# Kernel tuning notes

Hardware: AMD Instinct MI355X
Metric: run time of the kernel (lower is better)

Reference implementation:

```python
import jax, jax.numpy as jnp
import numpy as np

NBIT = 8


def _qmm(x, W, key):
    """Bit-serial quantized matmul with per-bit noisy weights (faithful to torch quantization()).
    x: (..., in), W: (out, in). Returns z (..., out), min, max, last noisy weight."""
    nsplit = 2 ** NBIT - 1
    mn = jnp.min(x)
    mx = jnp.max(x)
    q = ((x - mn) / (mx - mn) * nsplit).astype(jnp.uint8)  # trunc cast like torch .type(uint8)
    z = jnp.zeros(x.shape[:-1] + (W.shape[0],), x.dtype)
    Wn = W
    for i in range(NBIT):  # fixed 8-bit loop
        noise = jax.random.normal(jax.random.fold_in(key, i), W.shape, W.dtype) * jnp.abs(W) * 0.1
        Wn = W + noise
        bit = ((q >> i) & 1).astype(x.dtype) * float(2 ** i)
        z = z + jnp.matmul(bit, Wn.T)
    return z, mn, mx, Wn  # Wn = weight left in fc after loop (last bit's noisy weight)


def _requant(z, mn, mx, W_last):
    nsplit = 2 ** NBIT - 1
    bias = jnp.sum(mn * W_last, axis=1)  # (out,)
    return z / nsplit * (mx - mn) + bias


def _bn(x2d, gamma, beta, eps=1e-5):
    m = x2d.mean(axis=0)
    v = x2d.var(axis=0)  # biased, like torch BN training normalization
    return (x2d - m) / jnp.sqrt(v + eps) * gamma + beta


def _forward(node_embedding, edge_embedding, nbr_mask, c_two, c_two2, c_three, c_three2,
             bn2_g, bn2_b, bn3_g, bn3_b, nbr_idx):
    B, At, Nbr, Fe = edge_embedding.shape
    Fn = node_embedding.shape[-1]
    gather = jax.vmap(lambda x, i: x[i])  # batched fancy gather along atom axis
    key = jax.random.key(42)

    # two-body
    node_i = jnp.broadcast_to(node_embedding[:, :, None, :], (B, At, Nbr, Fn))
    node_j = gather(node_embedding, nbr_idx) * nbr_mask[..., None]  # (B,At,Nbr,Fn)
    c2 = jnp.concatenate([node_i, node_j], axis=3)  # (B,At,Nbr,2Fn)
    z, mn, mx, Wl = _qmm(c2, c_two, jax.random.fold_in(key, 0))
    c2 = jax.nn.relu(_requant(z, mn, mx, Wl))
    z, mn, mx, Wl = _qmm(c2, c_two2, jax.random.fold_in(key, 1))
    c2 = _requant(z, mn, mx, Wl)
    g2, e2 = jnp.split(c2, 2, axis=3)
    two = jax.nn.sigmoid(g2) * jnp.tanh(e2)
    two = _bn(two.reshape(-1, Fe), bn2_g, bn2_b).reshape(B, At, Nbr, Fe)

    # three-body
    nbr_jk = gather(nbr_idx, nbr_idx)                 # (B,At,Nbr,Nbr) neighbors-of-neighbors
    node_k = gather(node_embedding, nbr_jk)           # (B,At,Nbr,Nbr,Fn)
    edge_jk = gather(edge_embedding, nbr_idx)         # (B,At,Nbr,Nbr,Fe)
    edge_ij = jnp.broadcast_to(edge_embedding[:, :, :, None, :], (B, At, Nbr, Nbr, Fe))
    c3 = jnp.concatenate([
        jnp.broadcast_to(node_i[:, :, :, None, :], (B, At, Nbr, Nbr, Fn)),
        jnp.broadcast_to(node_j[:, :, :, None, :], (B, At, Nbr, Nbr, Fn)),
        node_k, edge_ij, edge_jk], axis=4)            # (B,At,Nbr,Nbr,3Fn+2Fe)
    z, mn, mx, Wl = _qmm(c3, c_three, jax.random.fold_in(key, 2))
    c3 = jax.nn.relu(_requant(z, mn, mx, Wl))
    z, mn, mx, Wl = _qmm(c3, c_three2, jax.random.fold_in(key, 3))
    c3 = _requant(z, mn, mx, Wl)
    g3, e3 = jnp.split(c3, 2, axis=4)
    three = jax.nn.sigmoid(g3) * jnp.tanh(e3)
    mask_jk = gather(nbr_mask, nbr_idx)               # (B,At,Nbr,Nbr) = nbr_mask[b, nbr_idx[b,i,j], k]
    three = (three * mask_jk[..., None]).sum(axis=3)  # (B,At,Nbr,Fe)
    three = _bn(three.reshape(-1, Fe), bn3_g, bn3_b).reshape(B, At, Nbr, Fe)

    return jax.nn.relu(edge_embedding + two + three)


def setup_inputs() -> dict:
    key = jax.random.key(0)
    ks = jax.random.split(key, 8)
    B, At, Nbr, Fn, Fe = 4, 48, 20, 64, 64
    return {
        "node_embedding": jax.random.normal(ks[0], (B, At, Fn), jnp.float32),
        "edge_embedding": jax.random.normal(ks[1], (B, At, Nbr, Fe), jnp.float32),
        "nbr_mask": jnp.ones((B, At, Nbr), jnp.float32),
        "c_two": jax.random.normal(ks[2], (8 * Fn, 2 * Fn), jnp.float32) * 0.05,
        "c_two2": jax.random.normal(ks[3], (2 * Fe, 8 * Fn), jnp.float32) * 0.05,
        "c_three": jax.random.normal(ks[4], (6 * Fn + 4 * Fe, 3 * Fn + 2 * Fe), jnp.float32) * 0.05,
        "c_three2": jax.random.normal(ks[5], (2 * Fe, 6 * Fn + 4 * Fe), jnp.float32) * 0.05,
        "bn2_g": jnp.ones((Fe,), jnp.float32),
        "bn2_b": jnp.zeros((Fe,), jnp.float32),
        "bn3_g": jnp.ones((Fe,), jnp.float32),
        "bn3_b": jnp.zeros((Fe,), jnp.float32),
        "nbr_idx": jax.random.randint(ks[6], (B, At, Nbr), 0, At, jnp.int32),
    }


def reference(node_embedding, edge_embedding, nbr_mask, c_two, c_two2, c_three, c_three2,
              bn2_g, bn2_b, bn3_g, bn3_b, nbr_idx):
    return _forward(node_embedding, edge_embedding, nbr_mask, c_two, c_two2, c_three, c_three2,
                    bn2_g, bn2_b, bn3_g, bn3_b, nbr_idx)
```

## Files before the change

### kernel.cpp

```cpp
#include <hip/hip_runtime.h>
#include <cstdint>
#include <cstddef>

#define DEVI __device__ __forceinline__

typedef __attribute__((ext_vector_type(8))) short s8v;
typedef __attribute__((ext_vector_type(4))) float f4v;

static constexpr int B_ = 4, AT = 48, NBRS = 20;
static constexpr int R2 = B_ * AT * NBRS;
static constexpr int M4 = R2 * NBRS;

static constexpr size_t OFF_B2A  = 0;
static constexpr size_t OFF_B2B  = OFF_B2A + 524288;
static constexpr size_t OFF_B3A  = OFF_B2B + 524288;
static constexpr size_t OFF_BW3B = OFF_B3A + 1638400;
static constexpr size_t OFF_BN3B = OFF_BW3B + 81920;
static constexpr size_t OFF_W72A = OFF_BN3B + 327680;
static constexpr size_t OFF_W72B = OFF_W72A + 65536;
static constexpr size_t OFF_W73A = OFF_W72B + 65536;
static constexpr size_t OFF_W73B = OFF_W73A + 204800;
static constexpr size_t OFF_RS   = OFF_W73B + 81920;
static constexpr size_t OFF_SLOT = OFF_RS + 1408;
static constexpr size_t OFF_BN   = OFF_SLOT + 16;
// ... 222 lines not shown
    unsigned char* __restrict__ Q2A, unsigned* __restrict__ slot4) {
  __shared__ float sred[512];
  int idx0 = blockIdx.x * 256 + threadIdx.x;
  if (idx0 < R2 * 128) {
    const float mn = o2f(slot0[0]), mx = o2f(slot0[1]);
    float invd = 255.f / (mx - mn);
    Q2A[idx0] = (unsigned char)((c2in[idx0] - mn) * invd);
  }
  const int n0 = 12288, n1 = n0 + 245760, n2 = n1 + 245760, total = n2 + 4915200;
  float lmn = 3.4e38f, lmx = -3.4e38f;
  for (int idx = idx0; idx < total; idx += gridDim.x * 256) {
    float v, v2;
    if (idx < n0) { v = node[idx]; v2 = v; }
    else if (idx < n1) { v = edge[idx - n0]; v2 = v; }
    else if (idx < n2) {
      int j = idx - n1; int r = j >> 6, c = j & 63;
      v = c2in[(size_t)r * 128 + 64 + c]; v2 = v;
    } else {
      int j = idx - n2; int bij = j / 1280, t = j - bij * 1280;
      int b = bij / 960;
      size_t base = (size_t)((b * 48 + nidx[bij]) * 20) * 64 + t;
      v = NK[base]; v2 = edge[base];
    }
    lmn = fminf(lmn, fminf(v, v2)); lmx = fmaxf(lmx, fmaxf(v, v2));
  }
  blockMinMax(lmn, lmx, sred, slot4);
}

__global__ __launch_bounds__(256) void k_mfma_gemm(
    const unsigned char* __restrict__ Q, int ldq,
    const short* __restrict__ B, int KGfull, int kg0,
    int M, int Nfull, int KB, float* __restrict__ Z, int accflag) {
  const int tid = threadIdx.x;
  const int lane = tid & 63, wave = tid >> 6;
  const int wr = wave >> 1, wc = wave & 1;
  const int l15 = lane & 15, l4 = lane >> 4;
  const int mbase = blockIdx.y * 128 + wr * 64;
  const int nbase = blockIdx.x * 128 + wc * 64;
  const int kq0 = blockIdx.z * KB;
  f4v acc[4][4];
  #pragma unroll
  for (int a = 0; a < 4; ++a)
    #pragma unroll
    for (int b = 0; b < 4; ++b) acc[a][b] = f4v{0.f, 0.f, 0.f, 0.f};
  for (int ks16 = 0; ks16 < KB; ks16 += 16) {
    uint4 qv[4];
    #pragma unroll
    for (int mf = 0; mf < 4; ++mf) {
      int row = mbase + mf * 16 + l15; if (row >= M) row = M - 1;
      qv[mf] = *(const uint4*)(Q + (size_t)row * ldq + kq0 + ks16);
    }
    #pragma unroll
    for (int sub = 0; sub < 4; ++sub) {
      int kg = kg0 + ((kq0 + ks16) >> 2) + sub;
      s8v af[4];
      #pragma unroll
      for (int mf = 0; mf < 4; ++mf) {
        unsigned w = (sub == 0) ? qv[mf].x : (sub == 1) ? qv[mf].y : (sub == 2) ? qv[mf].z : qv[mf].w;
        af[mf] = expand_mul((w >> (l4 * 8)) & 255u);
      }
      #pragma unroll
      for (int nf = 0; nf < 4; ++nf) {
        size_t o = (((size_t)(nbase / 16 + nf) * KGfull + kg) * 2) * 512 + (size_t)lane * 8;
        s8v bh = *(const s8v*)(B + o);
        s8v bl = *(const s8v*)(B + o + 512);
        #pragma unroll
        for (int mf = 0; mf < 4; ++mf) {
          acc[mf][nf] = __builtin_amdgcn_mfma_f32_16x16x32_bf16(af[mf], bh, acc[mf][nf], 0, 0, 0);
          acc[mf][nf] = __builtin_amdgcn_mfma_f32_16x16x32_bf16(af[mf], bl, acc[mf][nf], 0, 0, 0);
        }
      }
    }
  }
  #pragma unroll
  for (int mf = 0; mf < 4; ++mf) {
    #pragma unroll
    for (int r = 0; r < 4; ++r) {
      int m = mbase + mf * 16 + l4 * 4 + r;
      if (m >= M) continue;
      float* zp = Z + (size_t)m * Nfull + nbase;
      #pragma unroll
      for (int nf = 0; nf < 4; ++nf) {
        int n = nf * 16 + l15;
        if (accflag == 0) zp[n] = acc[mf][nf][r];
        else atomicAdd(zp + n, acc[mf][nf][r]);
      }
    }
  }
}

__global__ __launch_bounds__(256) void k_act1(const float* __restrict__ z1, const float* __restrict__ rs,
                                              const unsigned* __restrict__ slot0, float* __restrict__ c2b,
                                              unsigned* __restrict__ slot1) {
  __shared__ float sred[512];
  const float mn = o2f(slot0[0]), mx = o2f(slot0[1]);
  int idx = blockIdx.x * 256 + threadIdx.x;
  float lmn = 3.4e38f, lmx = -3.4e38f;
  if (idx < R2 * 512) {
    int o = idx & 511;
    float v = fmaxf(0.f, z1[idx] * (1.f / 255.f) * (mx - mn) + mn * rs[o]);
    c2b[idx] = v; lmn = v; lmx = v;
  }
  blockMinMax(lmn, lmx, sred, slot1);
}

__global__ __launch_bounds__(256) void k_qq(
    const float* __restrict__ c2b, const float* __restrict__ node, const float* __restrict__ edge,
    const float* __restrict__ c2in, const float* __restrict__ NK,
    const int* __restrict__ nidx, const unsigned* __restrict__ slot2, const unsigned* __restrict__ slot4,
    unsigned char* __restrict__ Q2B, unsigned char* __restrict__ QP2, unsigned char* __restrict__ QP3) {
  int idx = blockIdx.x * 256 + threadIdx.x;
  if (idx < R2 * 512) {
    const float mn = o2f(slot2[0]), mx = o2f(slot2[1]);
    Q2B[idx] = (unsigned char)((c2b[idx] - mn) * (255.f / (mx - mn)));
    return;
  }
  int j = idx - R2 * 512;
  const int seg = 245760;
  if (j >= 5 * seg) return;
  const float mn = o2f(slot4[0]), mx = o2f(slot4[1]);
  const float invd = 255.f / (mx - mn);
  int s = j / seg; int jj = j - s * seg;
  int r = jj >> 6, c = jj & 63;
  float v; unsigned char* dst;
  if (s == 0)      { v = node[(size_t)(r / 20) * 64 + c];  dst = QP2 + (size_t)r * 192 + c; }
  else if (s == 1) { v = c2in[(size_t)r * 128 + 64 + c];   dst = QP2 + (size_t)r * 192 + 64 + c; }
  else if (s == 2) { v = edge[(size_t)r * 64 + c];         dst = QP2 + (size_t)r * 192 + 128 + c; }
  else if (s == 3) { v = NK[(size_t)r * 64 + c];           dst = QP3 + (size_t)r * 128 + c; }
  else             { v = edge[(size_t)r * 64 + c];         dst = QP3 + (size_t)r * 128 + 64 + c; }
  *dst = (unsigned char)((v - mn) * invd);
}

__global__ __launch_bounds__(256) void k_mfma_p23(
    const unsigned char* __restrict__ Q2, const unsigned char* __restrict__ Q3,
    const short* __restrict__ B, float* __restrict__ P2, float* __restrict__ P3) {
  const int half = blockIdx.y >= 30;
  const int by = blockIdx.y - half * 30;
  const unsigned char* Q = half ? Q3 : Q2;
  float* Z = half ? P3 : P2;
  const int kg0 = half ? 48 : 0;
  const int KB = half ? 128 : 192;
  const int ldq = half ? 128 : 192;
  const int tid = threadIdx.x;
  const int lane = tid & 63, wave = tid >> 6;
  const int wr = wave >> 1, wc = wave & 1;
  const int l15 = lane & 15, l4 = lane >> 4;
  const int mbase = by * 128 + wr * 64;
  const int nbase = blockIdx.x * 128 + wc * 64;
  f4v acc[4][4];
  #pragma unroll
  for (int a = 0; a < 4; ++a)
    #pragma unroll
    for (int b = 0; b < 4; ++b) acc[a][b] = f4v{0.f, 0.f, 0.f, 0.f};
  for (int ks16 = 0; ks16 < KB; ks16 += 16) {
    uint4 qv[4];
    #pragma unroll
    for (int mf = 0; mf < 4; ++mf)
      qv[mf] = *(const uint4*)(Q + (size_t)(mbase + mf * 16 + l15) * ldq + ks16);
    #pragma unroll
    for (int sub = 0; sub < 4; ++sub) {
      int kg = kg0 + (ks16 >> 2) + sub;
      s8v af[4];
      #pragma unroll
      for (int mf = 0; mf < 4; ++mf) {
        unsigned w = (sub == 0) ? qv[mf].x : (sub == 1) ? qv[mf].y : (sub == 2) ? qv[mf].z : qv[mf].w;
        af[mf] = expand_mul((w >> (l4 * 8)) & 255u);
      }
      #pragma unroll
      for (int nf = 0; nf < 4; ++nf) {
        size_t o = (((size_t)(nbase / 16 + nf) * 80 + kg) * 2) * 512 + (size_t)lane * 8;
        s8v bh = *(const s8v*)(B + o);
        s8v bl = *(const s8v*)(B + o + 512);
        #pragma unroll
        for (int mf = 0; mf < 4; ++mf) {
          acc[mf][nf] = __builtin_amdgcn_mfma_f32_16x16x32_bf16(af[mf], bh, acc[mf][nf], 0, 0, 0);
          acc[mf][nf] = __builtin_amdgcn_mfma_f32_16x16x32_bf16(af[mf], bl, acc[mf][nf], 0, 0, 0);
        }
      }
    }
  }
  #pragma unroll
  for (int mf = 0; mf < 4; ++mf) {
    #pragma unroll
    for (int r = 0; r < 4; ++r) {
      int m = mbase + mf * 16 + l4 * 4 + r;
      float* zp = Z + (size_t)m * 640 + nbase;
      #pragma unroll
      for (int nf = 0; nf < 4; ++nf)
        zp[nf * 16 + l15] = acc[mf][nf][r];
    }
  }
}

__global__ __launch_bounds__(256) void k_act2mm3(
    const float* __restrict__ z2, const float* __restrict__ rs2b,
    const unsigned* __restrict__ slot2, float* __restrict__ two,
    const float* __restrict__ P12, const float* __restrict__ P3,
    const float* __restrict__ rs3a, const int* __restrict__ nidx,
    const unsigned* __restrict__ slot4, unsigned* __restrict__ slot6) {
  __shared__ float p12s[640];
  __shared__ float bias[640];
  __shared__ float sred[512];
  int gid = blockIdx.x * 256 + threadIdx.x;
  if (gid < R2 * 64) {
    const float mn = o2f(slot2[0]), mx = o2f(slot2[1]);
    int row = gid >> 6, c = gid & 63;
    float d = (mx - mn) * (1.f / 255.f);
    float g = z2[(size_t)row * 128 + c] * d + mn * rs2b[c];
    float e = z2[(size_t)row * 128 + 64 + c] * d + mn * rs2b[64 + c];
    two[gid] = (1.f / (1.f + expf(-g))) * tanhf(e);
  }
  const int bij = blockIdx.x;
  const int b = bij / 960;
  const int jp = nidx[bij];
  const size_t p3b = (size_t)((b * 48 + jp) * 20) * 640;
  const float mn2 = o2f(slot4[0]), mx2 = o2f(slot4[1]);
  const float sc2 = (mx2 - mn2) * (1.f / 255.f);
  for (int k = threadIdx.x; k < 640; k += 256) {
    p12s[k] = P12[(size_t)bij * 640 + k];
    bias[k] = mn2 * rs3a[k];
  }
  __syncthreads();
  float lmn = 3.4e38f, lmx = -3.4e38f;
  for (int t = threadIdx.x; t < 20 * 640; t += 256) {
    int knb = t / 640, k = t - knb * 640;
    float v = fmaxf(0.f, (p12s[k] + P3[p3b + t]) * sc2 + bias[k]);
    lmn = fminf(lmn, v); lmx = fmaxf(lmx, v);
  }
  blockMinMax(lmn, lmx, sred, slot6);
}

__global__ __launch_bounds__(256) void k_mfma_l3b(
    const float* __restrict__ P12, const float* __restrict__ P3,
    const float* __restrict__ rs3a, const float* __restrict__ rs3b,
    const short* __restrict__ BW, const short* __restrict__ BN,
    const int* __restrict__ nidx, const float* __restrict__ mask,
    const unsigned* __restrict__ slotA, const unsigned* __restrict__ slotB,
    float* __restrict__ tsum) {
  __shared__ unsigned char qt[64 * 648];
  __shared__ float bias[640];
  const int tid = threadIdx.x;
  const int s0 = blockIdx.x * 64;
  const float mn2 = o2f(slotA[0]), mx2 = o2f(slotA[1]);
  const float mn3 = o2f(slotB[0]), mx3 = o2f(slotB[1]);
  const float sc2 = (mx2 - mn2) * (1.f / 255.f);
  const float invd3 = 255.f / (mx3 - mn3);
  for (int k = tid; k < 640; k += 256) bias[k] = mn2 * rs3a[k];
  __syncthreads();
  {
    int r = tid >> 2, kq = (tid & 3) * 160;
    int s = s0 + r;
    int bij = s / 20, knb = s - bij * 20, b = bij / 960;
    int p3row = (b * 48 + nidx[bij]) * 20 + knb;
    const float* pa = P12 + (size_t)bij * 640;
    const float* pb = P3 + (size_t)p3row * 640;
    for (int k = kq; k < kq + 160; k += 4) {
      float4 va = *(const float4*)(pa + k);
      float4 vb = *(const float4*)(pb + k);
      float v0 = fmaxf(0.f, (va.x + vb.x) * sc2 + bias[k + 0]);
      float v1 = fmaxf(0.f, (va.y + vb.y) * sc2 + bias[k + 1]);
      float v2 = fmaxf(0.f, (va.z + vb.z) * sc2 + bias[k + 2]);
      float v3 = fmaxf(0.f, (va.w + vb.w) * sc2 + bias[k + 3]);
      unsigned pk = (unsigned)((v0 - mn3) * invd3) | ((unsigned)((v1 - mn3) * invd3) << 8)
                  | ((unsigned)((v2 - mn3) * invd3) << 16) | ((unsigned)((v3 - mn3) * invd3) << 24);
      *(unsigned*)(&qt[(size_t)r * 648 + k]) = pk;
    }
  }
  __syncthreads();
  const int lane = tid & 63, wave = tid >> 6;
  const int wm = wave >> 1, wn = wave & 1;
  const int l15 = lane & 15, l4 = lane >> 4;
  const int nfl[4] = {2 * wn, 2 * wn + 1, 2 * wn + 4, 2 * wn + 5};
  size_t bb[4];
  #pragma unroll
  for (int j = 0; j < 4; ++j) bb[j] = ((size_t)nfl[j] * 160) * 512 + (size_t)lane * 8;
  f4v acc[2][4];
  #pragma unroll
  for (int a = 0; a < 2; ++a)
    #pragma unroll
    for (int b = 0; b < 4; ++b) acc[a][b] = f4v{0.f, 0.f, 0.f, 0.f};
  s8v cb[4];
  #pragma unroll
  for (int j = 0; j < 4; ++j) cb[j] = *(const s8v*)(BN + bb[j]);
  const unsigned char* qrow0 = &qt[(size_t)(wm * 32 + l15) * 648];
  const unsigned char* qrow1 = qrow0 + 16 * 648;
  for (int c = 0; c < 20; ++c) {
    #pragma unroll
    for (int s = 0; s < 8; ++s) {
      const int kg = c * 8 + s;
      unsigned w0 = *(const unsigned*)(qrow0 + kg * 4);
      unsigned w1 = *(const unsigned*)(qrow1 + kg * 4);
      s8v af0 = expand_mul((w0 >> (l4 * 8)) & 255u);
      s8v af1 = expand_mul((w1 >> (l4 * 8)) & 255u);
      s8v nb[4];
      #pragma unroll
      for (int j = 0; j < 4; ++j)
        nb[j] = *(const s8v*)(BN + bb[j] + (size_t)(kg + 1) * 512);
      #pragma unroll
      for (int j = 0; j < 4; ++j) {
        acc[0][j] = __builtin_amdgcn_mfma_f32_16x16x32_bf16(af0, cb[j], acc[0][j], 0, 0, 0);
        acc[1][j] = __builtin_amdgcn_mfma_f32_16x16x32_bf16(af1, cb[j], acc[1][j], 0, 0, 0);
      }
      #pragma unroll
      for (int j = 0; j < 4; ++j) cb[j] = nb[j];
    }
    {
      unsigned a0 = *(const unsigned*)(qrow0 + c * 32 + l4 * 8);
      unsigned a1 = *(const unsigned*)(qrow0 + c * 32 + l4 * 8 + 4);
      s8v aq0 = bytes_to_bf16(a0, a1);
      a0 = *(const unsigned*)(qrow1 + c * 32 + l4 * 8);
      a1 = *(const unsigned*)(qrow1 + c * 32 + l4 * 8 + 4);
      s8v aq1 = bytes_to_bf16(a0, a1);
      #pragma unroll
      for (int j = 0; j < 4; ++j) {
        #pragma unroll
        for (int h = 0; h < 2; ++h) {
          s8v bw = *(const s8v*)(BW + (((size_t)nfl[j] * 20 + c) * 2 + h) * 512 + (size_t)lane * 8);
          acc[0][j] = __builtin_amdgcn_mfma_f32_16x16x32_bf16(aq0, bw, acc[0][j], 0, 0, 0);
          acc[1][j] = __builtin_amdgcn_mfma_f32_16x16x32_bf16(aq1, bw, acc[1][j], 0, 0, 0);
        }
      }
    }
  }
  const float d3 = (mx3 - mn3) * (1.f / 255.f);
  float rg[2], re[2];
  #pragma unroll
  for (int j = 0; j < 2; ++j) {
    int gcol = (2 * wn + j) * 16 + l15;
    rg[j] = mn3 * rs3b[gcol];
    re[j] = mn3 * rs3b[64 + gcol];
  }
  #pragma unroll
  for (int mf = 0; mf < 2; ++mf) {
    #pragma unroll
    for (int r = 0; r < 4; ++r) {
      int s = s0 + wm * 32 + mf * 16 + l4 * 4 + r;
      int bij = s / 20, knb = s - bij * 20, b = bij / 960;
      int p3row = (b * 48 + nidx[bij]) * 20 + knb;
      float mk = mask[p3row];
      #pragma unroll
      for (int j = 0; j < 2; ++j) {
        float g = acc[mf][j][r] * d3 + rg[j];
        float e = acc[mf][j + 2][r] * d3 + re[j];
        float val = (1.f / (1.f + expf(-g))) * tanhf(e) * mk;
        atomicAdd(&tsum[(size_t)bij * 64 + (2 * wn + j) * 16 + l15], val);
      }
    }
  }
}

__global__ __launch_bounds__(256) void k_bnstats2(const float* __restrict__ two, const float* __restrict__ tsum,
                                                  float* __restrict__ bn) {
  __shared__ float ss[512];
  const float* x = blockIdx.y ? tsum : two;
  float* mout = bn + (blockIdx.y ? 128 : 0);
  float* vout = mout + 64;
  int c = blockIdx.x, t = threadIdx.x;
  float s = 0.f, q = 0.f;
  for (int r = t; r < R2; r += 256) { float v = x[(size_t)r * 64 + c]; s += v; q += v * v; }
  ss[t] = s; ss[256 + t] = q;
  __syncthreads();
  for (int st = 128; st > 0; st >>= 1) {
    if (t < st) { ss[t] += ss[t + st]; ss[256 + t] += ss[256 + t + st]; }
    __syncthreads();
  }
  if (t == 0) { float m = ss[0] / (float)R2; mout[c] = m; vout[c] = ss[256] / (float)R2 - m * m; }
}

__global__ __launch_bounds__(256) void k_final(const float* __restrict__ edge, const float* __restrict__ two,
                                               const float* __restrict__ tsum, const float* __restrict__ bn,
                                               const float* __restrict__ g2, const float* __restrict__ b2,
                                               const float* __restrict__ g3, const float* __restrict__ b3,
                                               float* __restrict__ out) {
  int idx = blockIdx.x * 256 + threadIdx.x;
  if (idx >= R2 * 64) return;
  int c = idx & 63;
  float t2 = (two[idx] - bn[c]) / sqrtf(bn[64 + c] + 1e-5f) * g2[c] + b2[c];
  float t3 = (tsum[idx] - bn[128 + c]) / sqrtf(bn[192 + c] + 1e-5f) * g3[c] + b3[c];
  out[idx] = fmaxf(0.f, edge[idx] + t2 + t3);
// ... 8 lines not shown
  const float* mask   = (const float*)d_in[2];
  const float* c_two  = (const float*)d_in[3];
  const float* c_two2 = (const float*)d_in[4];
  const float* c_three  = (const float*)d_in[5];
  const float* c_three2 = (const float*)d_in[6];
  const float* bn2g = (const float*)d_in[7];
  const float* bn2b = (const float*)d_in[8];
  const float* bn3g = (const float*)d_in[9];
  const float* bn3b = (const float*)d_in[10];
  const int*   nidx = (const int*)d_in[11];
  float* ws = (float*)d_ws;
  unsigned* slots = (unsigned*)(ws + OFF_SLOT);
  float* out = (float*)d_out;
  short* B2A  = (short*)(ws + OFF_B2A);
  short* B2B  = (short*)(ws + OFF_B2B);
  short* B3A  = (short*)(ws + OFF_B3A);
  short* BW3B = (short*)(ws + OFF_BW3B);
  short* BN3B = (short*)(ws + OFF_BN3B);
  unsigned char* Q2A = (unsigned char*)(ws + OFF_Q2A);
  unsigned char* Q2B = (unsigned char*)(ws + OFF_Q2B);
  unsigned char* QP2 = (unsigned char*)(ws + OFF_QP2);
  unsigned char* QP3 = (unsigned char*)(ws + OFF_QP3);
  float* RS = ws + OFF_RS;

  k_prep<<<13056, 256, 0, stream>>>(c_two, c_two2, c_three, c_three2,
                                    B2A, B2B, B3A, BW3B, BN3B,
                                    ws + OFF_W72A, ws + OFF_W72B, ws + OFF_W73A, ws + OFF_W73B,
                                    ws + OFF_Z1, ws + OFF_Z2, ws + OFF_TSUM, slots);
  k_build2<<<2886, 256, 0, stream>>>(node, mask, nidx, ws + OFF_C2IN, ws + OFF_NK,
                                     ws + OFF_W72A, ws + OFF_W72B, ws + OFF_W73A, ws + OFF_W73B,
                                     RS, slots + 0);
  k_qm4<<<2048, 256, 0, stream>>>(node, edge, ws + OFF_C2IN, ws + OFF_NK, nidx, slots + 0,
                                  Q2A, slots + 4);
  k_mfma_gemm<<<dim3(4, 30, 2), 256, 0, stream>>>(Q2A, 128, B2A, 32, 0, 3840, 512, 64, ws + OFF_Z1, 3);
  k_act1<<<7680, 256, 0, stream>>>(ws + OFF_Z1, RS, slots + 0, ws + OFF_C2B, slots + 2);
  k_qq<<<12480, 256, 0, stream>>>(ws + OFF_C2B, node, edge, ws + OFF_C2IN, ws + OFF_NK,
                                  nidx, slots + 2, slots + 4, Q2B, QP2, QP3);
  k_mfma_gemm<<<dim3(1, 30, 4), 256, 0, stream>>>(Q2B, 512, B2B, 128, 0, 3840, 128, 128, ws + OFF_Z2, 3);
  k_mfma_p23<<<dim3(5, 60), 256, 0, stream>>>(QP2, QP3, B3A, ws + OFF_P2, ws + OFF_P3);
  k_act2mm3<<<3840, 256, 0, stream>>>(ws + OFF_Z2, RS + 512, slots + 2, ws + OFF_TWO,
                                      ws + OFF_P2, ws + OFF_P3, RS + 640, nidx, slots + 4, slots + 6);
  k_mfma_l3b<<<1200, 256, 0, stream>>>(ws + OFF_P2, ws + OFF_P3, RS + 640, RS + 1280,
                                       BW3B, BN3B, nidx, mask, slots + 4, slots + 6, ws + OFF_TSUM);
  k_bnstats2<<<dim3(64, 2), 256, 0, stream>>>(ws + OFF_TWO, ws + OFF_TSUM, ws + OFF_BN);
  k_final<<<960, 256, 0, stream>>>(edge, ws + OFF_TWO, ws + OFF_TSUM, ws + OFF_BN,
                                   bn2g, bn2b, bn3g, bn3b, out);
}
```

Baseline: 846.7 us.

## Halve GEMM M-tiles, swizzle LDS in l3b, and deepen B-fragment prefetch

The generic and p23 MFMA GEMMs shrink from 128-row to 64-row block tiles with doubled grid y, so more blocks are launched on the many CUs at small M (3840). The M-bound clamp is dropped because 3840 divides evenly by 64. In k_mfma_l3b the padded 648-byte LDS rows are replaced by 640-byte rows with an XOR swizzle to avoid bank conflicts. The bias shared array is replaced by direct reads of rs3a, and B fragments are now prefetched two steps ahead, with the high W halves hoisted per chunk. Smaller tiles reduce reuse of each loaded B fragment and add more global B traffic per output.

```diff
diff --git a/kernel.cpp b/kernel.cpp
--- a/kernel.cpp
+++ b/kernel.cpp
@@ -281,27 +281,25 @@
   const int lane = tid & 63, wave = tid >> 6;
   const int wr = wave >> 1, wc = wave & 1;
   const int l15 = lane & 15, l4 = lane >> 4;
-  const int mbase = blockIdx.y * 128 + wr * 64;
+  const int mbase = blockIdx.y * 64 + wr * 32;
   const int nbase = blockIdx.x * 128 + wc * 64;
   const int kq0 = blockIdx.z * KB;
-  f4v acc[4][4];
-  #pragma unroll
-  for (int a = 0; a < 4; ++a)
+  f4v acc[2][4];
+  #pragma unroll
+  for (int a = 0; a < 2; ++a)
     #pragma unroll
     for (int b = 0; b < 4; ++b) acc[a][b] = f4v{0.f, 0.f, 0.f, 0.f};
   for (int ks16 = 0; ks16 < KB; ks16 += 16) {
-    uint4 qv[4];
-    #pragma unroll
-    for (int mf = 0; mf < 4; ++mf) {
-      int row = mbase + mf * 16 + l15; if (row >= M) row = M - 1;
-      qv[mf] = *(const uint4*)(Q + (size_t)row * ldq + kq0 + ks16);
-    }
+    uint4 qv[2];
+    #pragma unroll
+    for (int mf = 0; mf < 2; ++mf)
+      qv[mf] = *(const uint4*)(Q + (size_t)(mbase + mf * 16 + l15) * ldq + kq0 + ks16);
     #pragma unroll
     for (int sub = 0; sub < 4; ++sub) {
       int kg = kg0 + ((kq0 + ks16) >> 2) + sub;
-      s8v af[4];
-      #pragma unroll
-      for (int mf = 0; mf < 4; ++mf) {
+      s8v af[2];
+      #pragma unroll
+      for (int mf = 0; mf < 2; ++mf) {
         unsigned w = (sub == 0) ? qv[mf].x : (sub == 1) ? qv[mf].y : (sub == 2) ? qv[mf].z : qv[mf].w;
         af[mf] = expand_mul((w >> (l4 * 8)) & 255u);
       }
@@ -311,7 +309,7 @@
         s8v bh = *(const s8v*)(B + o);
         s8v bl = *(const s8v*)(B + o + 512);
         #pragma unroll
-        for (int mf = 0; mf < 4; ++mf) {
+        for (int mf = 0; mf < 2; ++mf) {
           acc[mf][nf] = __builtin_amdgcn_mfma_f32_16x16x32_bf16(af[mf], bh, acc[mf][nf], 0, 0, 0);
           acc[mf][nf] = __builtin_amdgcn_mfma_f32_16x16x32_bf16(af[mf], bl, acc[mf][nf], 0, 0, 0);
         }
@@ -319,11 +317,10 @@
     }
   }
   #pragma unroll
-  for (int mf = 0; mf < 4; ++mf) {
+  for (int mf = 0; mf < 2; ++mf) {
     #pragma unroll
     for (int r = 0; r < 4; ++r) {
       int m = mbase + mf * 16 + l4 * 4 + r;
-      if (m >= M) continue;
       float* zp = Z + (size_t)m * Nfull + nbase;
       #pragma unroll
       for (int nf = 0; nf < 4; ++nf) {
@@ -380,8 +377,8 @@
 __global__ __launch_bounds__(256) void k_mfma_p23(
     const unsigned char* __restrict__ Q2, const unsigned char* __restrict__ Q3,
     const short* __restrict__ B, float* __restrict__ P2, float* __restrict__ P3) {
-  const int half = blockIdx.y >= 30;
-  const int by = blockIdx.y - half * 30;
+  const int half = blockIdx.y >= 60;
+  const int by = blockIdx.y - half * 60;
   const unsigned char* Q = half ? Q3 : Q2;
   float* Z = half ? P3 : P2;
   const int kg0 = half ? 48 : 0;
@@ -391,24 +388,24 @@
   const int lane = tid & 63, wave = tid >> 6;
   const int wr = wave >> 1, wc = wave & 1;
   const int l15 = lane & 15, l4 = lane >> 4;
-  const int mbase = by * 128 + wr * 64;
+  const int mbase = by * 64 + wr * 32;
   const int nbase = blockIdx.x * 128 + wc * 64;
-  f4v acc[4][4];
-  #pragma unroll
-  for (int a = 0; a < 4; ++a)
+  f4v acc[2][4];
+  #pragma unroll
+  for (int a = 0; a < 2; ++a)
     #pragma unroll
     for (int b = 0; b < 4; ++b) acc[a][b] = f4v{0.f, 0.f, 0.f, 0.f};
   for (int ks16 = 0; ks16 < KB; ks16 += 16) {
-    uint4 qv[4];
-    #pragma unroll
-    for (int mf = 0; mf < 4; ++mf)
+    uint4 qv[2];
+    #pragma unroll
+    for (int mf = 0; mf < 2; ++mf)
       qv[mf] = *(const uint4*)(Q + (size_t)(mbase + mf * 16 + l15) * ldq + ks16);
     #pragma unroll
     for (int sub = 0; sub < 4; ++sub) {
       int kg = kg0 + (ks16 >> 2) + sub;
-      s8v af[4];
-      #pragma unroll
-      for (int mf = 0; mf < 4; ++mf) {
+      s8v af[2];
+      #pragma unroll
+      for (int mf = 0; mf < 2; ++mf) {
         unsigned w = (sub == 0) ? qv[mf].x : (sub == 1) ? qv[mf].y : (sub == 2) ? qv[mf].z : qv[mf].w;
         af[mf] = expand_mul((w >> (l4 * 8)) & 255u);
       }
@@ -418,7 +415,7 @@
         s8v bh = *(const s8v*)(B + o);
         s8v bl = *(const s8v*)(B + o + 512);
         #pragma unroll
-        for (int mf = 0; mf < 4; ++mf) {
+        for (int mf = 0; mf < 2; ++mf) {
           acc[mf][nf] = __builtin_amdgcn_mfma_f32_16x16x32_bf16(af[mf], bh, acc[mf][nf], 0, 0, 0);
           acc[mf][nf] = __builtin_amdgcn_mfma_f32_16x16x32_bf16(af[mf], bl, acc[mf][nf], 0, 0, 0);
         }
@@ -426,7 +423,7 @@
     }
   }
   #pragma unroll
-  for (int mf = 0; mf < 4; ++mf) {
+  for (int mf = 0; mf < 2; ++mf) {
     #pragma unroll
     for (int r = 0; r < 4; ++r) {
       int m = mbase + mf * 16 + l4 * 4 + r;
@@ -483,16 +480,13 @@
     const int* __restrict__ nidx, const float* __restrict__ mask,
     const unsigned* __restrict__ slotA, const unsigned* __restrict__ slotB,
     float* __restrict__ tsum) {
-  __shared__ unsigned char qt[64 * 648];
-  __shared__ float bias[640];
+  __shared__ unsigned char qt[64 * 640];
   const int tid = threadIdx.x;
   const int s0 = blockIdx.x * 64;
   const float mn2 = o2f(slotA[0]), mx2 = o2f(slotA[1]);
   const float mn3 = o2f(slotB[0]), mx3 = o2f(slotB[1]);
   const float sc2 = (mx2 - mn2) * (1.f / 255.f);
   const float invd3 = 255.f / (mx3 - mn3);
-  for (int k = tid; k < 640; k += 256) bias[k] = mn2 * rs3a[k];
-  __syncthreads();
   {
     int r = tid >> 2, kq = (tid & 3) * 160;
     int s = s0 + r;
@@ -500,16 +494,18 @@
     int p3row = (b * 48 + nidx[bij]) * 20 + knb;
     const float* pa = P12 + (size_t)bij * 640;
     const float* pb = P3 + (size_t)p3row * 640;
+    const int swr = (r & 7) << 2;
     for (int k = kq; k < kq + 160; k += 4) {
       float4 va = *(const float4*)(pa + k);
       float4 vb = *(const float4*)(pb + k);
-      float v0 = fmaxf(0.f, (va.x + vb.x) * sc2 + bias[k + 0]);
-      float v1 = fmaxf(0.f, (va.y + vb.y) * sc2 + bias[k + 1]);
-      float v2 = fmaxf(0.f, (va.z + vb.z) * sc2 + bias[k + 2]);
-      float v3 = fmaxf(0.f, (va.w + vb.w) * sc2 + bias[k + 3]);
+      float4 rv = *(const float4*)(rs3a + k);
+      float v0 = fmaxf(0.f, (va.x + vb.x) * sc2 + mn2 * rv.x);
+      float v1 = fmaxf(0.f, (va.y + vb.y) * sc2 + mn2 * rv.y);
+      float v2 = fmaxf(0.f, (va.z + vb.z) * sc2 + mn2 * rv.z);
+      float v3 = fmaxf(0.f, (va.w + vb.w) * sc2 + mn2 * rv.w);
       unsigned pk = (unsigned)((v0 - mn3) * invd3) | ((unsigned)((v1 - mn3) * invd3) << 8)
                   | ((unsigned)((v2 - mn3) * invd3) << 16) | ((unsigned)((v3 - mn3) * invd3) << 24);
-      *(unsigned*)(&qt[(size_t)r * 648 + k]) = pk;
+      *(unsigned*)(&qt[(size_t)r * 640 + (k ^ swr)]) = pk;
     }
   }
   __syncthreads();
@@ -517,6 +513,10 @@
   const int wm = wave >> 1, wn = wave & 1;
   const int l15 = lane & 15, l4 = lane >> 4;
   const int nfl[4] = {2 * wn, 2 * wn + 1, 2 * wn + 4, 2 * wn + 5};
+  const int row0 = wm * 32 + l15;
+  const int sw = (row0 & 7) << 2;
+  const unsigned char* qb0 = qt + (size_t)row0 * 640;
+  const unsigned char* qb1 = qb0 + 16 * 640;
   size_t bb[4];
   #pragma unroll
   for (int j = 0; j < 4; ++j) bb[j] = ((size_t)nfl[j] * 160) * 512 + (size_t)lane * 8;
@@ -525,46 +525,51 @@
   for (int a = 0; a < 2; ++a)
     #pragma unroll
     for (int b = 0; b < 4; ++b) acc[a][b] = f4v{0.f, 0.f, 0.f, 0.f};
-  s8v cb[4];
-  #pragma unroll
-  for (int j = 0; j < 4; ++j) cb[j] = *(const s8v*)(BN + bb[j]);
-  const unsigned char* qrow0 = &qt[(size_t)(wm * 32 + l15) * 648];
-  const unsigned char* qrow1 = qrow0 + 16 * 648;
+  s8v c0[4], c1[4];
+  #pragma unroll
+  for (int j = 0; j < 4; ++j) {
+    c0[j] = *(const s8v*)(BN + bb[j]);
+    c1[j] = *(const s8v*)(BN + bb[j] + 512);
+  }
   for (int c = 0; c < 20; ++c) {
+    s8v bwh[4];
+    #pragma unroll
+    for (int j = 0; j < 4; ++j)
+      bwh[j] = *(const s8v*)(BW + (((size_t)nfl[j] * 20 + c) * 2) * 512 + (size_t)lane * 8);
     #pragma unroll
     for (int s = 0; s < 8; ++s) {
       const int kg = c * 8 + s;
-      unsigned w0 = *(const unsigned*)(qrow0 + kg * 4);
-      unsigned w1 = *(const unsigned*)(qrow1 + kg * 4);
+      unsigned w0 = *(const unsigned*)(qb0 + ((kg * 4) ^ sw));
+      unsigned w1 = *(const unsigned*)(qb1 + ((kg * 4) ^ sw));
       s8v af0 = expand_mul((w0 >> (l4 * 8)) & 255u);
       s8v af1 = expand_mul((w1 >> (l4 * 8)) & 255u);
-      s8v nb[4];
+      s8v nx[4];
       #pragma unroll
       for (int j = 0; j < 4; ++j)
-        nb[j] = *(const s8v*)(BN + bb[j] + (size_t)(kg + 1) * 512);
+        nx[j] = *(const s8v*)(BN + bb[j] + (size_t)(kg + 2) * 512);
       #pragma unroll
       for (int j = 0; j < 4; ++j) {
-        acc[0][j] = __builtin_amdgcn_mfma_f32_16x16x32_bf16(af0, cb[j], acc[0][j], 0, 0, 0);
-        acc[1][j] = __builtin_amdgcn_mfma_f32_16x16x32_bf16(af1, cb[j], acc[1][j], 0, 0, 0);
-      }
-      #pragma unroll
-      for (int j = 0; j < 4; ++j) cb[j] = nb[j];
+        acc[0][j] = __builtin_amdgcn_mfma_f32_16x16x32_bf16(af0, c0[j], acc[0][j], 0, 0, 0);
+        acc[1][j] = __builtin_amdgcn_mfma_f32_16x16x32_bf16(af1, c0[j], acc[1][j], 0, 0, 0);
+      }
+      #pragma unroll
+      for (int j = 0; j < 4; ++j) { c0[j] = c1[j]; c1[j] = nx[j]; }
     }
     {
-      unsigned a0 = *(const unsigned*)(qrow0 + c * 32 + l4 * 8);
-      unsigned a1 = *(const unsigned*)(qrow0 + c * 32 + l4 * 8 + 4);
+      const int x = c * 32 + l4 * 8;
+      unsigned a0 = *(const unsigned*)(qb0 + (x ^ sw));
+      unsigned a1 = *(const unsigned*)(qb0 + ((x + 4) ^ sw));
       s8v aq0 = bytes_to_bf16(a0, a1);
-      a0 = *(const unsigned*)(qrow1 + c * 32 + l4 * 8);
-      a1 = *(const unsigned*)(qrow1 + c * 32 + l4 * 8 + 4);
+      a0 = *(const unsigned*)(qb1 + (x ^ sw));
+      a1 = *(const unsigned*)(qb1 + ((x + 4) ^ sw));
       s8v aq1 = bytes_to_bf16(a0, a1);
       #pragma unroll
       for (int j = 0; j < 4; ++j) {
-        #pragma unroll
-        for (int h = 0; h < 2; ++h) {
-          s8v bw = *(const s8v*)(BW + (((size_t)nfl[j] * 20 + c) * 2 + h) * 512 + (size_t)lane * 8);
-          acc[0][j] = __builtin_amdgcn_mfma_f32_16x16x32_bf16(aq0, bw, acc[0][j], 0, 0, 0);
-          acc[1][j] = __builtin_amdgcn_mfma_f32_16x16x32_bf16(aq1, bw, acc[1][j], 0, 0, 0);
-        }
+        acc[0][j] = __builtin_amdgcn_mfma_f32_16x16x32_bf16(aq0, bwh[j], acc[0][j], 0, 0, 0);
+        acc[1][j] = __builtin_amdgcn_mfma_f32_16x16x32_bf16(aq1, bwh[j], acc[1][j], 0, 0, 0);
+        s8v bwl = *(const s8v*)(BW + ((((size_t)nfl[j] * 20 + c) * 2) + 1) * 512 + (size_t)lane * 8);
+        acc[0][j] = __builtin_amdgcn_mfma_f32_16x16x32_bf16(aq0, bwl, acc[0][j], 0, 0, 0);
+        acc[1][j] = __builtin_amdgcn_mfma_f32_16x16x32_bf16(aq1, bwl, acc[1][j], 0, 0, 0);
       }
     }
   }
@@ -665,12 +670,12 @@
                                      RS, slots + 0);
   k_qm4<<<2048, 256, 0, stream>>>(node, edge, ws + OFF_C2IN, ws + OFF_NK, nidx, slots + 0,
                                   Q2A, slots + 4);
-  k_mfma_gemm<<<dim3(4, 30, 2), 256, 0, stream>>>(Q2A, 128, B2A, 32, 0, 3840, 512, 64, ws + OFF_Z1, 3);
+  k_mfma_gemm<<<dim3(4, 60, 2), 256, 0, stream>>>(Q2A, 128, B2A, 32, 0, 3840, 512, 64, ws + OFF_Z1, 3);
   k_act1<<<7680, 256, 0, stream>>>(ws + OFF_Z1, RS, slots + 0, ws + OFF_C2B, slots + 2);
   k_qq<<<12480, 256, 0, stream>>>(ws + OFF_C2B, node, edge, ws + OFF_C2IN, ws + OFF_NK,
                                   nidx, slots + 2, slots + 4, Q2B, QP2, QP3);
-  k_mfma_gemm<<<dim3(1, 30, 4), 256, 0, stream>>>(Q2B, 512, B2B, 128, 0, 3840, 128, 128, ws + OFF_Z2, 3);
-  k_mfma_p23<<<dim3(5, 60), 256, 0, stream>>>(QP2, QP3, B3A, ws + OFF_P2, ws + OFF_P3);
+  k_mfma_gemm<<<dim3(1, 60, 4), 256, 0, stream>>>(Q2B, 512, B2B, 128, 0, 3840, 128, 128, ws + OFF_Z2, 3);
+  k_mfma_p23<<<dim3(5, 120), 256, 0, stream>>>(QP2, QP3, B3A, ws + OFF_P2, ws + OFF_P3);
   k_act2mm3<<<3840, 256, 0, stream>>>(ws + OFF_Z2, RS + 512, slots + 2, ws + OFF_TWO,
                                       ws + OFF_P2, ws + OFF_P3, RS + 640, nidx, slots + 4, slots + 6);
   k_mfma_l3b<<<1200, 256, 0, stream>>>(ws + OFF_P2, ws + OFF_P3, RS + 640, RS + 1280,
```

Result: slower. 883.3 us (+4.3%).

## Retile MFMA GEMMs to 64-row blocks and recompute activation instead of storing

Applied to the files above, without the earlier changes.

The generic and p23 MFMA GEMMs now use 64x128 block tiles, with each wave owning 64 rows and 32 columns, and twice as many blocks are launched to give more parallelism. k_act1 no longer writes the ReLU activation buffer, and k_qq recomputes it from Z1 so one full float write and read are avoided. k_mfma_l3b is restructured so each wave handles all 64 rows with two N-fragments, the shared bias table is dropped, and B operands are double-buffered two steps ahead. The cost is recomputing the activation, more total B-operand loads across blocks, and removal of the M bound checks.

```diff
diff --git a/kernel.cpp b/kernel.cpp
--- a/kernel.cpp
+++ b/kernel.cpp
@@ -278,42 +278,39 @@
     const short* __restrict__ B, int KGfull, int kg0,
     int M, int Nfull, int KB, float* __restrict__ Z, int accflag) {
   const int tid = threadIdx.x;
-  const int lane = tid & 63, wave = tid >> 6;
-  const int wr = wave >> 1, wc = wave & 1;
+  const int lane = tid & 63, w = tid >> 6;
   const int l15 = lane & 15, l4 = lane >> 4;
-  const int mbase = blockIdx.y * 128 + wr * 64;
-  const int nbase = blockIdx.x * 128 + wc * 64;
+  const int mbase = blockIdx.y * 64;
+  const int nbase = blockIdx.x * 128;
   const int kq0 = blockIdx.z * KB;
-  f4v acc[4][4];
+  f4v acc[4][2];
   #pragma unroll
   for (int a = 0; a < 4; ++a)
     #pragma unroll
-    for (int b = 0; b < 4; ++b) acc[a][b] = f4v{0.f, 0.f, 0.f, 0.f};
+    for (int b = 0; b < 2; ++b) acc[a][b] = f4v{0.f, 0.f, 0.f, 0.f};
   for (int ks16 = 0; ks16 < KB; ks16 += 16) {
     uint4 qv[4];
     #pragma unroll
-    for (int mf = 0; mf < 4; ++mf) {
-      int row = mbase + mf * 16 + l15; if (row >= M) row = M - 1;
-      qv[mf] = *(const uint4*)(Q + (size_t)row * ldq + kq0 + ks16);
-    }
+    for (int mf = 0; mf < 4; ++mf)
+      qv[mf] = *(const uint4*)(Q + (size_t)(mbase + mf * 16 + l15) * ldq + kq0 + ks16);
     #pragma unroll
     for (int sub = 0; sub < 4; ++sub) {
       int kg = kg0 + ((kq0 + ks16) >> 2) + sub;
       s8v af[4];
       #pragma unroll
       for (int mf = 0; mf < 4; ++mf) {
-        unsigned w = (sub == 0) ? qv[mf].x : (sub == 1) ? qv[mf].y : (sub == 2) ? qv[mf].z : qv[mf].w;
-        af[mf] = expand_mul((w >> (l4 * 8)) & 255u);
-      }
-      #pragma unroll
-      for (int nf = 0; nf < 4; ++nf) {
-        size_t o = (((size_t)(nbase / 16 + nf) * KGfull + kg) * 2) * 512 + (size_t)lane * 8;
+        unsigned wv = (sub == 0) ? qv[mf].x : (sub == 1) ? qv[mf].y : (sub == 2) ? qv[mf].z : qv[mf].w;
+        af[mf] = expand_mul((wv >> (l4 * 8)) & 255u);
+      }
+      #pragma unroll
+      for (int j = 0; j < 2; ++j) {
+        size_t o = (((size_t)(nbase / 16 + w * 2 + j) * KGfull + kg) * 2) * 512 + (size_t)lane * 8;
         s8v bh = *(const s8v*)(B + o);
         s8v bl = *(const s8v*)(B + o + 512);
         #pragma unroll
         for (int mf = 0; mf < 4; ++mf) {
-          acc[mf][nf] = __builtin_amdgcn_mfma_f32_16x16x32_bf16(af[mf], bh, acc[mf][nf], 0, 0, 0);
-          acc[mf][nf] = __builtin_amdgcn_mfma_f32_16x16x32_bf16(af[mf], bl, acc[mf][nf], 0, 0, 0);
+          acc[mf][j] = __builtin_amdgcn_mfma_f32_16x16x32_bf16(af[mf], bh, acc[mf][j], 0, 0, 0);
+          acc[mf][j] = __builtin_amdgcn_mfma_f32_16x16x32_bf16(af[mf], bl, acc[mf][j], 0, 0, 0);
         }
       }
     }
@@ -323,20 +320,19 @@
     #pragma unroll
     for (int r = 0; r < 4; ++r) {
       int m = mbase + mf * 16 + l4 * 4 + r;
-      if (m >= M) continue;
       float* zp = Z + (size_t)m * Nfull + nbase;
       #pragma unroll
-      for (int nf = 0; nf < 4; ++nf) {
-        int n = nf * 16 + l15;
-        if (accflag == 0) zp[n] = acc[mf][nf][r];
-        else atomicAdd(zp + n, acc[mf][nf][r]);
+      for (int j = 0; j < 2; ++j) {
+        int n = (w * 2 + j) * 16 + l15;
+        if (accflag == 0) zp[n] = acc[mf][j][r];
+        else atomicAdd(zp + n, acc[mf][j][r]);
       }
     }
   }
 }
 
 __global__ __launch_bounds__(256) void k_act1(const float* __restrict__ z1, const float* __restrict__ rs,
-                                              const unsigned* __restrict__ slot0, float* __restrict__ c2b,
+                                              const unsigned* __restrict__ slot0,
                                               unsigned* __restrict__ slot1) {
   __shared__ float sred[512];
   const float mn = o2f(slot0[0]), mx = o2f(slot0[1]);
@@ -345,20 +341,25 @@
   if (idx < R2 * 512) {
     int o = idx & 511;
     float v = fmaxf(0.f, z1[idx] * (1.f / 255.f) * (mx - mn) + mn * rs[o]);
-    c2b[idx] = v; lmn = v; lmx = v;
+    lmn = v; lmx = v;
   }
   blockMinMax(lmn, lmx, sred, slot1);
 }
 
 __global__ __launch_bounds__(256) void k_qq(
-    const float* __restrict__ c2b, const float* __restrict__ node, const float* __restrict__ edge,
+    const float* __restrict__ z1, const float* __restrict__ rs,
+    const float* __restrict__ node, const float* __restrict__ edge,
     const float* __restrict__ c2in, const float* __restrict__ NK,
-    const int* __restrict__ nidx, const unsigned* __restrict__ slot2, const unsigned* __restrict__ slot4,
+    const int* __restrict__ nidx, const unsigned* __restrict__ slot0,
+    const unsigned* __restrict__ slot2, const unsigned* __restrict__ slot4,
     unsigned char* __restrict__ Q2B, unsigned char* __restrict__ QP2, unsigned char* __restrict__ QP3) {
   int idx = blockIdx.x * 256 + threadIdx.x;
   if (idx < R2 * 512) {
+    const float mn0 = o2f(slot0[0]), mx0 = o2f(slot0[1]);
     const float mn = o2f(slot2[0]), mx = o2f(slot2[1]);
-    Q2B[idx] = (unsigned char)((c2b[idx] - mn) * (255.f / (mx - mn)));
+    int o = idx & 511;
+    float v = fmaxf(0.f, z1[idx] * (1.f / 255.f) * (mx0 - mn0) + mn0 * rs[o]);
+    Q2B[idx] = (unsigned char)((v - mn) * (255.f / (mx - mn)));
     return;
   }
   int j = idx - R2 * 512;
@@ -380,24 +381,23 @@
 __global__ __launch_bounds__(256) void k_mfma_p23(
     const unsigned char* __restrict__ Q2, const unsigned char* __restrict__ Q3,
     const short* __restrict__ B, float* __restrict__ P2, float* __restrict__ P3) {
-  const int half = blockIdx.y >= 30;
-  const int by = blockIdx.y - half * 30;
+  const int half = blockIdx.y >= 60;
+  const int by = blockIdx.y - half * 60;
   const unsigned char* Q = half ? Q3 : Q2;
   float* Z = half ? P3 : P2;
   const int kg0 = half ? 48 : 0;
   const int KB = half ? 128 : 192;
   const int ldq = half ? 128 : 192;
   const int tid = threadIdx.x;
-  const int lane = tid & 63, wave = tid >> 6;
-  const int wr = wave >> 1, wc = wave & 1;
+  const int lane = tid & 63, w = tid >> 6;
   const int l15 = lane & 15, l4 = lane >> 4;
-  const int mbase = by * 128 + wr * 64;
-  const int nbase = blockIdx.x * 128 + wc * 64;
-  f4v acc[4][4];
+  const int mbase = by * 64;
+  const int nbase = blockIdx.x * 128;
+  f4v acc[4][2];
   #pragma unroll
   for (int a = 0; a < 4; ++a)
     #pragma unroll
-    for (int b = 0; b < 4; ++b) acc[a][b] = f4v{0.f, 0.f, 0.f, 0.f};
+    for (int b = 0; b < 2; ++b) acc[a][b] = f4v{0.f, 0.f, 0.f, 0.f};
   for (int ks16 = 0; ks16 < KB; ks16 += 16) {
     uint4 qv[4];
     #pragma unroll
@@ -409,18 +409,18 @@
       s8v af[4];
       #pragma unroll
       for (int mf = 0; mf < 4; ++mf) {
-        unsigned w = (sub == 0) ? qv[mf].x : (sub == 1) ? qv[mf].y : (sub == 2) ? qv[mf].z : qv[mf].w;
-        af[mf] = expand_mul((w >> (l4 * 8)) & 255u);
-      }
-      #pragma unroll
-      for (int nf = 0; nf < 4; ++nf) {
-        size_t o = (((size_t)(nbase / 16 + nf) * 80 + kg) * 2) * 512 + (size_t)lane * 8;
+        unsigned wv = (sub == 0) ? qv[mf].x : (sub == 1) ? qv[mf].y : (sub == 2) ? qv[mf].z : qv[mf].w;
+        af[mf] = expand_mul((wv >> (l4 * 8)) & 255u);
+      }
+      #pragma unroll
+      for (int j = 0; j < 2; ++j) {
+        size_t o = (((size_t)(nbase / 16 + w * 2 + j) * 80 + kg) * 2) * 512 + (size_t)lane * 8;
         s8v bh = *(const s8v*)(B + o);
         s8v bl = *(const s8v*)(B + o + 512);
         #pragma unroll
         for (int mf = 0; mf < 4; ++mf) {
-          acc[mf][nf] = __builtin_amdgcn_mfma_f32_16x16x32_bf16(af[mf], bh, acc[mf][nf], 0, 0, 0);
-          acc[mf][nf] = __builtin_amdgcn_mfma_f32_16x16x32_bf16(af[mf], bl, acc[mf][nf], 0, 0, 0);
+          acc[mf][j] = __builtin_amdgcn_mfma_f32_16x16x32_bf16(af[mf], bh, acc[mf][j], 0, 0, 0);
+          acc[mf][j] = __builtin_amdgcn_mfma_f32_16x16x32_bf16(af[mf], bl, acc[mf][j], 0, 0, 0);
         }
       }
     }
@@ -432,8 +432,8 @@
       int m = mbase + mf * 16 + l4 * 4 + r;
       float* zp = Z + (size_t)m * 640 + nbase;
       #pragma unroll
-      for (int nf = 0; nf < 4; ++nf)
-        zp[nf * 16 + l15] = acc[mf][nf][r];
+      for (int j = 0; j < 2; ++j)
+        zp[(w * 2 + j) * 16 + l15] = acc[mf][j][r];
     }
   }
 }
@@ -484,15 +484,12 @@
     const unsigned* __restrict__ slotA, const unsigned* __restrict__ slotB,
     float* __restrict__ tsum) {
   __shared__ unsigned char qt[64 * 648];
-  __shared__ float bias[640];
   const int tid = threadIdx.x;
   const int s0 = blockIdx.x * 64;
   const float mn2 = o2f(slotA[0]), mx2 = o2f(slotA[1]);
   const float mn3 = o2f(slotB[0]), mx3 = o2f(slotB[1]);
   const float sc2 = (mx2 - mn2) * (1.f / 255.f);
   const float invd3 = 255.f / (mx3 - mn3);
-  for (int k = tid; k < 640; k += 256) bias[k] = mn2 * rs3a[k];
-  __syncthreads();
   {
     int r = tid >> 2, kq = (tid & 3) * 160;
     int s = s0 + r;
@@ -503,94 +500,91 @@
     for (int k = kq; k < kq + 160; k += 4) {
       float4 va = *(const float4*)(pa + k);
       float4 vb = *(const float4*)(pb + k);
-      float v0 = fmaxf(0.f, (va.x + vb.x) * sc2 + bias[k + 0]);
-      float v1 = fmaxf(0.f, (va.y + vb.y) * sc2 + bias[k + 1]);
-      float v2 = fmaxf(0.f, (va.z + vb.z) * sc2 + bias[k + 2]);
-      float v3 = fmaxf(0.f, (va.w + vb.w) * sc2 + bias[k + 3]);
+      float4 rv = *(const float4*)(rs3a + k);
+      float v0 = fmaxf(0.f, (va.x + vb.x) * sc2 + mn2 * rv.x);
+      float v1 = fmaxf(0.f, (va.y + vb.y) * sc2 + mn2 * rv.y);
+      float v2 = fmaxf(0.f, (va.z + vb.z) * sc2 + mn2 * rv.z);
+      float v3 = fmaxf(0.f, (va.w + vb.w) * sc2 + mn2 * rv.w);
       unsigned pk = (unsigned)((v0 - mn3) * invd3) | ((unsigned)((v1 - mn3) * invd3) << 8)
                   | ((unsigned)((v2 - mn3) * invd3) << 16) | ((unsigned)((v3 - mn3) * invd3) << 24);
       *(unsigned*)(&qt[(size_t)r * 648 + k]) = pk;
     }
   }
   __syncthreads();
-  const int lane = tid & 63, wave = tid >> 6;
-  const int wm = wave >> 1, wn = wave & 1;
+  const int lane = tid & 63, w = tid >> 6;
   const int l15 = lane & 15, l4 = lane >> 4;
-  const int nfl[4] = {2 * wn, 2 * wn + 1, 2 * wn + 4, 2 * wn + 5};
-  size_t bb[4];
-  #pragma unroll
-  for (int j = 0; j < 4; ++j) bb[j] = ((size_t)nfl[j] * 160) * 512 + (size_t)lane * 8;
-  f4v acc[2][4];
-  #pragma unroll
-  for (int a = 0; a < 2; ++a)
-    #pragma unroll
-    for (int b = 0; b < 4; ++b) acc[a][b] = f4v{0.f, 0.f, 0.f, 0.f};
-  s8v cb[4];
-  #pragma unroll
-  for (int j = 0; j < 4; ++j) cb[j] = *(const s8v*)(BN + bb[j]);
-  const unsigned char* qrow0 = &qt[(size_t)(wm * 32 + l15) * 648];
-  const unsigned char* qrow1 = qrow0 + 16 * 648;
+  const int nf0 = w, nf1 = w + 4;
+  const unsigned char* qr[4];
+  #pragma unroll
+  for (int mf = 0; mf < 4; ++mf) qr[mf] = qt + (size_t)(mf * 16 + l15) * 648;
+  const size_t bb0 = (size_t)nf0 * 160 * 512 + (size_t)lane * 8;
+  const size_t bb1 = (size_t)nf1 * 160 * 512 + (size_t)lane * 8;
+  f4v acc[4][2];
+  #pragma unroll
+  for (int a = 0; a < 4; ++a)
+    #pragma unroll
+    for (int b = 0; b < 2; ++b) acc[a][b] = f4v{0.f, 0.f, 0.f, 0.f};
+  s8v c00 = *(const s8v*)(BN + bb0), c01 = *(const s8v*)(BN + bb1);
+  s8v c10 = *(const s8v*)(BN + bb0 + 512), c11 = *(const s8v*)(BN + bb1 + 512);
   for (int c = 0; c < 20; ++c) {
+    s8v bwh0 = *(const s8v*)(BW + (((size_t)nf0 * 20 + c) * 2) * 512 + (size_t)lane * 8);
+    s8v bwh1 = *(const s8v*)(BW + (((size_t)nf1 * 20 + c) * 2) * 512 + (size_t)lane * 8);
     #pragma unroll
     for (int s = 0; s < 8; ++s) {
       const int kg = c * 8 + s;
-      unsigned w0 = *(const unsigned*)(qrow0 + kg * 4);
-      unsigned w1 = *(const unsigned*)(qrow1 + kg * 4);
-      s8v af0 = expand_mul((w0 >> (l4 * 8)) & 255u);
-      s8v af1 = expand_mul((w1 >> (l4 * 8)) & 255u);
-      s8v nb[4];
-      #pragma unroll
-      for (int j = 0; j < 4; ++j)
-        nb[j] = *(const s8v*)(BN + bb[j] + (size_t)(kg + 1) * 512);
-      #pragma unroll
-      for (int j = 0; j < 4; ++j) {
-        acc[0][j] = __builtin_amdgcn_mfma_f32_16x16x32_bf16(af0, cb[j], acc[0][j], 0, 0, 0);
-        acc[1][j] = __builtin_amdgcn_mfma_f32_16x16x32_bf16(af1, cb[j], acc[1][j], 0, 0, 0);
-      }
-      #pragma unroll
-      for (int j = 0; j < 4; ++j) cb[j] = nb[j];
+      s8v af[4];
+      #pragma unroll
+      for (int mf = 0; mf < 4; ++mf) {
+        unsigned wv = *(const unsigned*)(qr[mf] + kg * 4);
+        af[mf] = expand_mul((wv >> (l4 * 8)) & 255u);
+      }
+      s8v nx0 = *(const s8v*)(BN + bb0 + (size_t)(kg + 2) * 512);
+      s8v nx1 = *(const s8v*)(BN + bb1 + (size_t)(kg + 2) * 512);
+      #pragma unroll
+      for (int mf = 0; mf < 4; ++mf) {
+        acc[mf][0] = __builtin_amdgcn_mfma_f32_16x16x32_bf16(af[mf], c00, acc[mf][0], 0, 0, 0);
+        acc[mf][1] = __builtin_amdgcn_mfma_f32_16x16x32_bf16(af[mf], c01, acc[mf][1], 0, 0, 0);
+      }
+      c00 = c10; c01 = c11; c10 = nx0; c11 = nx1;
     }
     {
-      unsigned a0 = *(const unsigned*)(qrow0 + c * 32 + l4 * 8);
-      unsigned a1 = *(const unsigned*)(qrow0 + c * 32 + l4 * 8 + 4);
-      s8v aq0 = bytes_to_bf16(a0, a1);
-      a0 = *(const unsigned*)(qrow1 + c * 32 + l4 * 8);
-      a1 = *(const unsigned*)(qrow1 + c * 32 + l4 * 8 + 4);
-      s8v aq1 = bytes_to_bf16(a0, a1);
-      #pragma unroll
-      for (int j = 0; j < 4; ++j) {
-        #pragma unroll
-        for (int h = 0; h < 2; ++h) {
-          s8v bw = *(const s8v*)(BW + (((size_t)nfl[j] * 20 + c) * 2 + h) * 512 + (size_t)lane * 8);
-          acc[0][j] = __builtin_amdgcn_mfma_f32_16x16x32_bf16(aq0, bw, acc[0][j], 0, 0, 0);
-          acc[1][j] = __builtin_amdgcn_mfma_f32_16x16x32_bf16(aq1, bw, acc[1][j], 0, 0, 0);
-        }
+      s8v aq[4];
+      #pragma unroll
+      for (int mf = 0; mf < 4; ++mf) {
+        unsigned a0 = *(const unsigned*)(qr[mf] + c * 32 + l4 * 8);
+        unsigned a1 = *(const unsigned*)(qr[mf] + c * 32 + l4 * 8 + 4);
+        aq[mf] = bytes_to_bf16(a0, a1);
+      }
+      #pragma unroll
+      for (int mf = 0; mf < 4; ++mf) {
+        acc[mf][0] = __builtin_amdgcn_mfma_f32_16x16x32_bf16(aq[mf], bwh0, acc[mf][0], 0, 0, 0);
+        acc[mf][1] = __builtin_amdgcn_mfma_f32_16x16x32_bf16(aq[mf], bwh1, acc[mf][1], 0, 0, 0);
+      }
+      s8v bwl0 = *(const s8v*)(BW + ((((size_t)nf0 * 20 + c) * 2) + 1) * 512 + (size_t)lane * 8);
+      s8v bwl1 = *(const s8v*)(BW + ((((size_t)nf1 * 20 + c) * 2) + 1) * 512 + (size_t)lane * 8);
+      #pragma unroll
+      for (int mf = 0; mf < 4; ++mf) {
+        acc[mf][0] = __builtin_amdgcn_mfma_f32_16x16x32_bf16(aq[mf], bwl0, acc[mf][0], 0, 0, 0);
+        acc[mf][1] = __builtin_amdgcn_mfma_f32_16x16x32_bf16(aq[mf], bwl1, acc[mf][1], 0, 0, 0);
       }
     }
   }
   const float d3 = (mx3 - mn3) * (1.f / 255.f);
-  float rg[2], re[2];
-  #pragma unroll
-  for (int j = 0; j < 2; ++j) {
-    int gcol = (2 * wn + j) * 16 + l15;
-    rg[j] = mn3 * rs3b[gcol];
-    re[j] = mn3 * rs3b[64 + gcol];
-  }
-  #pragma unroll
-  for (int mf = 0; mf < 2; ++mf) {
+  const int col = w * 16 + l15;
+  const float rg = mn3 * rs3b[col];
+  const float re = mn3 * rs3b[64 + col];
+  #pragma unroll
+  for (int mf = 0; mf < 4; ++mf) {
     #pragma unroll
     for (int r = 0; r < 4; ++r) {
-      int s = s0 + wm * 32 + mf * 16 + l4 * 4 + r;
+      int s = s0 + mf * 16 + l4 * 4 + r;
       int bij = s / 20, knb = s - bij * 20, b = bij / 960;
       int p3row = (b * 48 + nidx[bij]) * 20 + knb;
       float mk = mask[p3row];
-      #pragma unroll
-      for (int j = 0; j < 2; ++j) {
-        float g = acc[mf][j][r] * d3 + rg[j];
-        float e = acc[mf][j + 2][r] * d3 + re[j];
-        float val = (1.f / (1.f + expf(-g))) * tanhf(e) * mk;
-        atomicAdd(&tsum[(size_t)bij * 64 + (2 * wn + j) * 16 + l15], val);
-      }
+      float g = acc[mf][0][r] * d3 + rg;
+      float e = acc[mf][1][r] * d3 + re;
+      float val = (1.f / (1.f + expf(-g))) * tanhf(e) * mk;
+      atomicAdd(&tsum[(size_t)bij * 64 + col], val);
     }
   }
 }
@@ -665,12 +659,12 @@
                                      RS, slots + 0);
   k_qm4<<<2048, 256, 0, stream>>>(node, edge, ws + OFF_C2IN, ws + OFF_NK, nidx, slots + 0,
                                   Q2A, slots + 4);
-  k_mfma_gemm<<<dim3(4, 30, 2), 256, 0, stream>>>(Q2A, 128, B2A, 32, 0, 3840, 512, 64, ws + OFF_Z1, 3);
-  k_act1<<<7680, 256, 0, stream>>>(ws + OFF_Z1, RS, slots + 0, ws + OFF_C2B, slots + 2);
-  k_qq<<<12480, 256, 0, stream>>>(ws + OFF_C2B, node, edge, ws + OFF_C2IN, ws + OFF_NK,
-                                  nidx, slots + 2, slots + 4, Q2B, QP2, QP3);
-  k_mfma_gemm<<<dim3(1, 30, 4), 256, 0, stream>>>(Q2B, 512, B2B, 128, 0, 3840, 128, 128, ws + OFF_Z2, 3);
-  k_mfma_p23<<<dim3(5, 60), 256, 0, stream>>>(QP2, QP3, B3A, ws + OFF_P2, ws + OFF_P3);
+  k_mfma_gemm<<<dim3(4, 60, 2), 256, 0, stream>>>(Q2A, 128, B2A, 32, 0, 3840, 512, 64, ws + OFF_Z1, 3);
+  k_act1<<<7680, 256, 0, stream>>>(ws + OFF_Z1, RS, slots + 0, slots + 2);
+  k_qq<<<12480, 256, 0, stream>>>(ws + OFF_Z1, RS, node, edge, ws + OFF_C2IN, ws + OFF_NK,
+                                  nidx, slots + 0, slots + 2, slots + 4, Q2B, QP2, QP3);
+  k_mfma_gemm<<<dim3(1, 60, 4), 256, 0, stream>>>(Q2B, 512, B2B, 128, 0, 3840, 128, 128, ws + OFF_Z2, 3);
+  k_mfma_p23<<<dim3(5, 120), 256, 0, stream>>>(QP2, QP3, B3A, ws + OFF_P2, ws + OFF_P3);
   k_act2mm3<<<3840, 256, 0, stream>>>(ws + OFF_Z2, RS + 512, slots + 2, ws + OFF_TWO,
                                       ws + OFF_P2, ws + OFF_P3, RS + 640, nidx, slots + 4, slots + 6);
   k_mfma_l3b<<<1200, 256, 0, stream>>>(ws + OFF_P2, ws + OFF_P3, RS + 640, RS + 1280,
```

After: 832.9 us. Within noise of the previous version (-1.6%).
